# Kernel optimization log

Measured on AMD Instinct MI355X. Metric: run time of the kernel, lower is better.

The kernel has to match this reference:

```python
import jax, jax.numpy as jnp
import numpy as np

H = 16   # num_heads
G = 4    # groups (code structurally requires 4)
DIM = 1024
HD = DIM // H // G  # 16


def setup_inputs() -> dict:
    key = jax.random.key(0)
    k1, k2, k3 = jax.random.split(key, 3)
    x = jax.random.normal(k1, (8, 4096, DIM), dtype=jnp.float32)
    w_qkvw = jax.random.normal(k2, (DIM, 4 * DIM), dtype=jnp.float32) * 0.02
    w_out = jax.random.normal(k3, (DIM, DIM), dtype=jnp.float32) * 0.02
    return {"x": x, "w_qkvw": w_qkvw, "w_out": w_out}


def reference(x, w_qkvw, w_out):
    B, S, dim = x.shape
    qkvw = x @ w_qkvw  # [B, S, 4*dim]
    # chunk into G groups along last dim -> G tensors of [B, S, dim] (G==4)
    chunks = jnp.split(qkvw, G, axis=-1)
    # each chunk split again into G sub-chunks of [B, S, dim/G]
    subs = [jnp.split(t, G, axis=-1) for t in chunks]
    # torch: q,k,v,w = [cat([qi,ki,vi,wi], dim=0) for qi,ki,vi,wi in zip(*subs)]
    q = jnp.concatenate([subs[i][0] for i in range(4)], axis=0)  # [4B, S, dim/G]
    k = jnp.concatenate([subs[i][1] for i in range(4)], axis=0)
    v = jnp.concatenate([subs[i][2] for i in range(4)], axis=0)
    w = jnp.concatenate([subs[i][3] for i in range(4)], axis=0)
    # faithful row-major reshape: [4B, S, dim/G] -> [4B, H, S, hd] -> transpose(1,2)
    def shp(t):
        return t.reshape(B * G, H, -1, HD).swapaxes(1, 2)  # [4B, S, H, hd]
    q, k, v = shp(q), shp(k), shp(v)
    w = w.reshape(B * G, H, -1, HD)  # [4B, H, S, hd]
    scale = HD ** -0.5
    scores = (q @ k.swapaxes(-2, -1)) * scale          # [4B, S, H, H]
    attn = jax.nn.softmax(scores, axis=-1)
    o = (attn @ v).swapaxes(1, 2).reshape(B, S, dim)   # [B, S, dim]
    return (o * w.reshape(B, S, dim)) @ w_out
```

## Files before the change

kernel.cpp:

```cpp
#include <hip/hip_runtime.h>
#include <hip/hip_bf16.h>
#include <stdint.h>


typedef __bf16 bf16;
typedef __bf16 bf16x8 __attribute__((ext_vector_type(8)));
typedef float f32x4 __attribute__((ext_vector_type(4)));

__device__ __forceinline__ void gload16(const bf16* g, bf16* l) {
  __builtin_amdgcn_global_load_lds(
      (const __attribute__((address_space(1))) void*)g,
      (__attribute__((address_space(3))) void*)l, 16, 0, 0);
}

#define BAR() asm volatile("s_barrier" ::: "memory")
#define SB() __builtin_amdgcn_sched_barrier(0)

#define READ_A(mq)                                                            \
  {                                                                           \
    _Pragma("unroll") for (int i = 0; i < 4; ++i)                             \
        _Pragma("unroll") for (int kk = 0; kk < 2; ++kk)                      \
            a[i][kk] = *(const bf16x8*)(lds + aoff +                          \
                                        ((mq)*64 + i * 16 + fr) * 128 +       \
                                        ((kk * 64 + fkb) ^ xo));              \
  }
#define READ_B(nh)                                                            \
  {                                                                           \
    _Pragma("unroll") for (int j = 0; j < 2; ++j)                             \
        _Pragma("unroll") for (int kk = 0; kk < 2; ++kk)                      \
            b[(nh)*2 + j][kk] = *(const bf16x8*)(lds + boff +                 \
                                                 (bro + (nh)*32 + j * 16 + fr) * 128 + \
                                                 ((kk * 64 + fkb) ^ xo));     \
  }
#define MFMA_Q(mq, nh)                                                        \
  {                                                                           \
    _Pragma("unroll") for (int i = 0; i < 4; ++i)                             \
        _Pragma("unroll") for (int j = 0; j < 2; ++j) {                       \
      acc[(mq)*4 + i][(nh)*2 + j] = __builtin_amdgcn_mfma_f32_16x16x32_bf16(  \
          a[i][0], b[(nh)*2 + j][0], acc[(mq)*4 + i][(nh)*2 + j], 0, 0, 0);   \
      acc[(mq)*4 + i][(nh)*2 + j] = __builtin_amdgcn_mfma_f32_16x16x32_bf16(  \
          a[i][1], b[(nh)*2 + j][1], acc[(mq)*4 + i][(nh)*2 + j], 0, 0, 0);   \
    }                                                                         \
  }
#define STAGE_A(h, X)                                                         \
  {                                                                           \
    const int ro = ((X)&1) * 65536 + (h)*16384;                               \
    const bf16* g = gA + ((h)*128) * 1024 + (X)*64;                           \
    gload16(g, (bf16*)(lds + ro + wv * 1024));                                \
    gload16(g + 64 * 1024, (bf16*)(lds + ro + 8192 + wv * 1024));             \
  }
#define STAGE_B(h, X)                                                         \
  {                                                                           \
    const int ro = ((X)&1) * 65536 + 32768 + (h)*16384;                       \
    const bf16* g = gB + ((h)*128) * 1024 + (X)*64;                           \
    gload16(g, (bf16*)(lds + ro + wv * 1024));                                \
    gload16(g + 64 * 1024, (bf16*)(lds + ro + 8192 + wv * 1024));             \
  }

template <typename OutT>
__global__ __launch_bounds__(512, 2)
void gemm256(const bf16* __restrict__ A, const bf16* __restrict__ BT,
             OutT* __restrict__ C, int N) {
  constexpr int K = 1024;
  __shared__ __align__(16) char smem[131072];
  char* lds = smem;

  const int tid = threadIdx.x;
  const int lane = tid & 63;
  const int wv = tid >> 6;
  const int wr = wv >> 2;
  const int wc = wv & 3;

  const int gx = gridDim.x;
  const int nwg = gx * gridDim.y;
  const int bid = blockIdx.y * gx + blockIdx.x;
  const int swz = (bid & 7) * (nwg >> 3) + (bid >> 3);
  const long row0 = (long)(swz / gx) * 256;
  const long col0 = (long)(swz % gx) * 256;

  const int srow = tid >> 3;
  const int scol = (((tid & 7) * 16) ^ ((srow & 7) << 4)) >> 1;
  const bf16* gA = A + (row0 + srow) * K + scol;
  const bf16* gB = BT + (col0 + srow) * K + scol;

  const int fr = lane & 15;
  const int fkb = (lane >> 4) * 16;
  const int xo = (fr & 7) << 4;
  const int bro = (wc & 1) * 64;

  bf16x8 a[4][2], b[4][2];
  f32x4 acc[8][4] = {};

  STAGE_A(0, 0); STAGE_A(1, 0); STAGE_B(0, 0); STAGE_B(1, 0);
  STAGE_B(0, 1); STAGE_B(1, 1);
  asm volatile("s_waitcnt vmcnt(4)" ::: "memory");
  SB(); BAR(); SB();

  for (int T = 0; T < 16; ++T) {
    const int d = T & 1;
    const int aoff = d * 65536 + wr * 16384;
    const int boff = d * 65536 + 32768 + (wc >> 1) * 16384;
    READ_A(0); READ_B(0);
    if (T < 15) STAGE_A(0, T + 1);
    SB(); BAR(); SB();
    __builtin_amdgcn_s_setprio(1); MFMA_Q(0, 0); __builtin_amdgcn_s_setprio(0);
    SB(); BAR(); SB();
    READ_B(1);
    if (T < 15) STAGE_A(1, T + 1);
    SB(); BAR(); SB();
    __builtin_amdgcn_s_setprio(1); MFMA_Q(0, 1); __builtin_amdgcn_s_setprio(0);
    SB(); BAR(); SB();
    READ_A(1);
    if (T < 14) STAGE_B(0, T + 2);
    SB(); BAR(); SB();
    __builtin_amdgcn_s_setprio(1); MFMA_Q(1, 0); __builtin_amdgcn_s_setprio(0);
    SB(); BAR(); SB();
    if (T < 14) {
      STAGE_B(1, T + 2);
      asm volatile("s_waitcnt vmcnt(4)" ::: "memory");
    } else if (T == 14) {
      asm volatile("s_waitcnt vmcnt(0)" ::: "memory");
    }
    SB(); BAR(); SB();
    __builtin_amdgcn_s_setprio(1); MFMA_Q(1, 1); __builtin_amdgcn_s_setprio(0);
    SB(); BAR(); SB();
  }

  const int crow = (lane >> 4) * 4;
  const int ccol = lane & 15;
  const long rb = row0 + wr * 128;
  const long cb = col0 + wc * 64;
#pragma unroll
  for (int m = 0; m < 8; ++m)
#pragma unroll
    for (int n = 0; n < 4; ++n)
#pragma unroll
      for (int i = 0; i < 4; ++i)
        C[(rb + m * 16 + crow + i) * (long)N + cb + n * 16 + ccol] =
            (OutT)acc[m][n][i];
}

__device__ __forceinline__ void load16f(const bf16* p, float* f) {
  const uint4* u = (const uint4*)p;
  uint4 a = u[0], b = u[1];
  uint32_t w[8] = {a.x, a.y, a.z, a.w, b.x, b.y, b.z, b.w};
#pragma unroll
  for (int j = 0; j < 8; ++j) {
    f[2 * j] = __uint_as_float(w[j] << 16);
    f[2 * j + 1] = __uint_as_float(w[j] & 0xffff0000u);
  }
}

__global__ __launch_bounds__(256)
void attn_fuse(const bf16* __restrict__ qkvw, bf16* __restrict__ ow,
               int b0, long bstride) {
  __shared__ bf16 data[16 * 1024];
  const int s_hi = blockIdx.x;
  const int g = blockIdx.y;
  const int bz = blockIdx.z;
  const int b = b0 + bz;
  const bf16* base = qkvw + (long)bz * bstride;
  const int tid = threadIdx.x;

#pragma unroll
  for (int i = 0; i < 8; ++i) {
    int c = tid + i * 256;
    int h = c >> 7;
    int col = (c & 127) * 8;
    *(uint4*)&data[h * 1024 + col] =
        *(const uint4*)(base + (long)(h * 256 + s_hi) * 4096 + g * 1024 + col);
  }
  __syncthreads();

  const int s_lo = tid >> 4;
  const int h1 = tid & 15;
  const int off = s_lo * 16;

  float q[16], p[16], o[16];
  load16f(&data[h1 * 1024 + off], q);

  float mx = -1e30f;
#pragma unroll
  for (int h2 = 0; h2 < 16; ++h2) {
    float kf[16];
    load16f(&data[h2 * 1024 + 256 + off], kf);
    float s = 0.f;
#pragma unroll
    for (int d = 0; d < 16; ++d) s += q[d] * kf[d];
    s *= 0.25f;
    p[h2] = s;
    mx = fmaxf(mx, s);
  }
  float sum = 0.f;
#pragma unroll
  for (int h2 = 0; h2 < 16; ++h2) {
    float e = __expf(p[h2] - mx);
    p[h2] = e;
    sum += e;
  }
  const float inv = 1.f / sum;
#pragma unroll
  for (int d = 0; d < 16; ++d) o[d] = 0.f;
#pragma unroll
  for (int h2 = 0; h2 < 16; ++h2) {
    float vf[16];
    load16f(&data[h2 * 1024 + 512 + off], vf);
    const float av = p[h2] * inv;
#pragma unroll
    for (int d = 0; d < 16; ++d) o[d] += av * vf[d];
  }
  float wf[16];
  load16f(&data[h1 * 1024 + 768 + off], wf);

  const int bp = g * 8 + b;
  const long R = (long)(bp >> 2) * 4096 + (bp & 3) * 1024 + h1 * 64 + (s_hi >> 2);
  const int cbo = (s_hi & 3) * 256 + off;
  union { uint4 u[2]; bf16 hh[16]; } st;
#pragma unroll
  for (int d = 0; d < 16; ++d) st.hh[d] = (bf16)(o[d] * wf[d]);
  uint4* dst = (uint4*)&ow[R * 1024 + cbo];
  dst[0] = st.u[0];
  dst[1] = st.u[1];
}

__global__ __launch_bounds__(256)
void cast_x_kernel(const float* __restrict__ in, bf16* __restrict__ out, long n4) {
  long i = (long)blockIdx.x * 256 + threadIdx.x;
  if (i >= n4) return;
  float4 v = ((const float4*)in)[i];
  union { uint2 d; bf16 h[4]; } r;
  r.h[0] = (bf16)v.x; r.h[1] = (bf16)v.y; r.h[2] = (bf16)v.z; r.h[3] = (bf16)v.w;
  ((uint2*)out)[i] = r.d;
}

__global__ __launch_bounds__(256)
void tcast_kernel(const float* __restrict__ in, bf16* __restrict__ out, int R, int C) {
  __shared__ float t[64][65];
  const int c0 = blockIdx.x * 64, r0 = blockIdx.y * 64;
  const int lr = threadIdx.x >> 6;
  const int lc = threadIdx.x & 63;
#pragma unroll
  for (int i = 0; i < 16; ++i)
    t[lr + i * 4][lc] = in[(long)(r0 + lr + i * 4) * C + c0 + lc];
  __syncthreads();
#pragma unroll
  for (int i = 0; i < 16; ++i) {
    int oc = lr + i * 4;
    out[(long)(c0 + oc) * R + r0 + lc] = (bf16)t[lc][oc];
  }
}

extern "C" void kernel_launch(void* const* d_in, const int* in_sizes, int n_in,
                              void* d_out, int out_size, void* d_ws, size_t ws_size,
                              hipStream_t stream) {
  const float* x = (const float*)d_in[0];
  const float* w_qkvw = (const float*)d_in[1];
  const float* w_out = (const float*)d_in[2];
  float* out = (float*)d_out;

  char* ws = (char*)d_ws;
  size_t off = 0;
  bf16* x_bf = (bf16*)(ws + off); off += (size_t)32768 * 1024 * 2;
  bf16* bt1  = (bf16*)(ws + off); off += (size_t)4096 * 1024 * 2;
  bf16* bt2  = (bf16*)(ws + off); off += (size_t)1024 * 1024 * 2;
  bf16* owb  = (bf16*)(ws + off); off += (size_t)32768 * 1024 * 2;
  bf16* qk   = (bf16*)(ws + off);
  const size_t rem = ws_size > off ? ws_size - off : 0;
  const size_t full_need = (size_t)32768 * 4096 * 2;

  cast_x_kernel<<<32768, 256, 0, stream>>>(x, x_bf, (long)8388608);
  tcast_kernel<<<dim3(64, 16), 256, 0, stream>>>(w_qkvw, bt1, 1024, 4096);
  tcast_kernel<<<dim3(16, 16), 256, 0, stream>>>(w_out, bt2, 1024, 1024);

  if (rem >= full_need) {
    gemm256<bf16><<<dim3(16, 128), 512, 0, stream>>>(x_bf, bt1, qk, 4096);
    attn_fuse<<<dim3(256, 4, 8), 256, 0, stream>>>(qk, owb, 0, (long)4096 * 4096);
  } else {
    for (int b = 0; b < 8; ++b) {
      gemm256<bf16><<<dim3(16, 16), 512, 0, stream>>>(
          x_bf + (size_t)b * 4096 * 1024, bt1, qk, 4096);
      attn_fuse<<<dim3(256, 4, 1), 256, 0, stream>>>(qk, owb, b, 0);
    }
  }
  gemm256<float><<<dim3(4, 128), 512, 0, stream>>>(owb, bt2, out, 1024);
}
```

Measured before the change: 478.4 us.

## Software-pipeline LDS reads across iterations and reorder GEMM phases

Restructures the 256x256 GEMM main loop so the first A/B fragment reads for the next tile are issued at the end of the current iteration, overlapping LDS reads with MFMA. It also cuts the barriers per iteration, reorders the MFMA quadrants, and makes the workgroup swizzle column-major over tiles. Epilogue stores become nontemporal to avoid polluting cache. The new ordering risks LDS read/write hazards between buffers and changes L2 reuse patterns.

```diff
diff --git a/kernel.cpp b/kernel.cpp
--- a/kernel.cpp
+++ b/kernel.cpp
@@ -13,22 +13,33 @@
       (__attribute__((address_space(3))) void*)l, 16, 0, 0);
 }
 
+__device__ __forceinline__ void nt_store(bf16 v, bf16* p) {
+  union { bf16 h; short s; } u; u.h = v;
+  __builtin_nontemporal_store(u.s, (short*)p);
+}
+__device__ __forceinline__ void nt_store(float v, float* p) {
+  __builtin_nontemporal_store(v, p);
+}
+
 #define BAR() asm volatile("s_barrier" ::: "memory")
 #define SB() __builtin_amdgcn_sched_barrier(0)
-
-#define READ_A(mq)                                                            \
+#define LGKM0 asm volatile("s_waitcnt lgkmcnt(0)" ::: "memory")
+#define PRIO1 __builtin_amdgcn_s_setprio(1)
+#define PRIO0 __builtin_amdgcn_s_setprio(0)
+
+#define READ_A(mq, AO)                                                        \
   {                                                                           \
     _Pragma("unroll") for (int i = 0; i < 4; ++i)                             \
         _Pragma("unroll") for (int kk = 0; kk < 2; ++kk)                      \
-            a[i][kk] = *(const bf16x8*)(lds + aoff +                          \
+            a[i][kk] = *(const bf16x8*)(lds + (AO) +                          \
                                         ((mq)*64 + i * 16 + fr) * 128 +       \
                                         ((kk * 64 + fkb) ^ xo));              \
   }
-#define READ_B(nh)                                                            \
+#define READ_B(nh, BO)                                                        \
   {                                                                           \
     _Pragma("unroll") for (int j = 0; j < 2; ++j)                             \
         _Pragma("unroll") for (int kk = 0; kk < 2; ++kk)                      \
-            b[(nh)*2 + j][kk] = *(const bf16x8*)(lds + boff +                 \
+            b[(nh)*2 + j][kk] = *(const bf16x8*)(lds + (BO) +                 \
                                                  (bro + (nh)*32 + j * 16 + fr) * 128 + \
                                                  ((kk * 64 + fkb) ^ xo));     \
   }
@@ -71,12 +82,12 @@
   const int wr = wv >> 2;
   const int wc = wv & 3;
 
-  const int gx = gridDim.x;
-  const int nwg = gx * gridDim.y;
-  const int bid = blockIdx.y * gx + blockIdx.x;
+  const int gy = gridDim.y;
+  const int nwg = gridDim.x * gy;
+  const int bid = blockIdx.y * gridDim.x + blockIdx.x;
   const int swz = (bid & 7) * (nwg >> 3) + (bid >> 3);
-  const long row0 = (long)(swz / gx) * 256;
-  const long col0 = (long)(swz % gx) * 256;
+  const long col0 = (long)(swz / gy) * 256;
+  const long row0 = (long)(swz % gy) * 256;
 
   const int srow = tid >> 3;
   const int scol = (((tid & 7) * 16) ^ ((srow & 7) << 4)) >> 1;
@@ -95,35 +106,38 @@
   STAGE_B(0, 1); STAGE_B(1, 1);
   asm volatile("s_waitcnt vmcnt(4)" ::: "memory");
   SB(); BAR(); SB();
+  {
+    const int aoff0 = wr * 16384;
+    const int boff0 = 32768 + (wc >> 1) * 16384;
+    READ_A(0, aoff0); READ_B(0, boff0);
+  }
+  SB();
 
   for (int T = 0; T < 16; ++T) {
     const int d = T & 1;
     const int aoff = d * 65536 + wr * 16384;
     const int boff = d * 65536 + 32768 + (wc >> 1) * 16384;
-    READ_A(0); READ_B(0);
-    if (T < 15) STAGE_A(0, T + 1);
-    SB(); BAR(); SB();
-    __builtin_amdgcn_s_setprio(1); MFMA_Q(0, 0); __builtin_amdgcn_s_setprio(0);
-    SB(); BAR(); SB();
-    READ_B(1);
-    if (T < 15) STAGE_A(1, T + 1);
-    SB(); BAR(); SB();
-    __builtin_amdgcn_s_setprio(1); MFMA_Q(0, 1); __builtin_amdgcn_s_setprio(0);
-    SB(); BAR(); SB();
-    READ_A(1);
-    if (T < 14) STAGE_B(0, T + 2);
-    SB(); BAR(); SB();
-    __builtin_amdgcn_s_setprio(1); MFMA_Q(1, 0); __builtin_amdgcn_s_setprio(0);
-    SB(); BAR(); SB();
+    const int aoffN = (d ^ 1) * 65536 + wr * 16384;
+    const int boffN = (d ^ 1) * 65536 + 32768 + (wc >> 1) * 16384;
+    if (T < 15) { STAGE_A(0, T + 1); STAGE_A(1, T + 1); }
+    SB(); BAR(); LGKM0; SB();
+    READ_B(1, boff); SB();
+    PRIO1; MFMA_Q(0, 0); PRIO0; SB();
+    BAR(); LGKM0; SB();
+    PRIO1; MFMA_Q(0, 1); PRIO0; SB();
+    READ_A(1, aoff); SB();
+    BAR(); LGKM0; SB();
+    PRIO1; MFMA_Q(1, 1); PRIO0; SB();
     if (T < 14) {
-      STAGE_B(1, T + 2);
+      STAGE_B(0, T + 2); STAGE_B(1, T + 2);
       asm volatile("s_waitcnt vmcnt(4)" ::: "memory");
     } else if (T == 14) {
       asm volatile("s_waitcnt vmcnt(0)" ::: "memory");
     }
-    SB(); BAR(); SB();
-    __builtin_amdgcn_s_setprio(1); MFMA_Q(1, 1); __builtin_amdgcn_s_setprio(0);
-    SB(); BAR(); SB();
+    SB(); BAR(); LGKM0; SB();
+    PRIO1; MFMA_Q(1, 0); PRIO0; SB();
+    if (T < 15) { READ_A(0, aoffN); READ_B(0, boffN); }
+    SB();
   }
 
   const int crow = (lane >> 4) * 4;
@@ -136,8 +150,8 @@
     for (int n = 0; n < 4; ++n)
 #pragma unroll
       for (int i = 0; i < 4; ++i)
-        C[(rb + m * 16 + crow + i) * (long)N + cb + n * 16 + ccol] =
-            (OutT)acc[m][n][i];
+        nt_store((OutT)acc[m][n][i],
+                 &C[(rb + m * 16 + crow + i) * (long)N + cb + n * 16 + ccol]);
 }
 
 __device__ __forceinline__ void load16f(const bf16* p, float* f) {
```

Result: slower. 528.2 us (+10.4%).
